# Kernel tuning notes

Measured on AMD Instinct MI355X. Metric: run time of the kernel, lower is better.

## Reference

```python
import jax, jax.numpy as jnp
import numpy as np

N = 4096
C = 8192
D = 64
MARGIN = 0.1
ALPHA = 32.0


def setup_inputs() -> dict:
    key = jax.random.key(0)
    k1, k2, k3, k4 = jax.random.split(key, 4)
    embeddings = jax.random.normal(k1, (N, D), dtype=jnp.float32)
    labels = jax.random.randint(k2, (N,), 0, C)
    # kaiming_normal_(mode='fan_out') on a (C, D) tensor -> std = sqrt(2/C)
    mean_proxies = jax.random.normal(k3, (C, D), dtype=jnp.float32) * np.sqrt(2.0 / C)
    log_variance_proxies = jax.random.normal(k4, (C, D), dtype=jnp.float32) * np.sqrt(2.0 / C)
    return {
        "embeddings": embeddings,
        "labels": labels,
        "mean_proxies": mean_proxies,
        "log_variance_proxies": log_variance_proxies,
    }


def _mls_scores(e, mu, logvar):
    """score[i,j] = -0.5 * sum_d[(e_id - mu_jd)^2 * exp(-logvar_jd) + logvar_jd].
    Expanded into GEMMs to avoid materializing the (N, C, D) broadcast tensor."""
    inv_var = jnp.exp(-logvar)                                  # (C, D)
    e2_term = (e * e) @ inv_var.T                               # (N, C)
    cross = e @ (mu * inv_var).T                                # (N, C)
    const = jnp.sum(mu * mu * inv_var + logvar, axis=1)         # (C,)
    return -0.5 * (e2_term - 2.0 * cross + const[None, :])      # (N, C)


def reference(embeddings, labels, mean_proxies, log_variance_proxies):
    score_mat = _mls_scores(embeddings, mean_proxies, log_variance_proxies)  # (N, C)
    pos_mask = jax.nn.one_hot(labels, C, dtype=score_mat.dtype)              # (N, C)

    pos_e = -ALPHA * (score_mat - MARGIN)
    neg_e = ALPHA * (score_mat + MARGIN)
    m = jnp.max(pos_e)  # NOTE: original code uses max(pos_exp) for BOTH terms
    pos_exp = jnp.exp(pos_e - m)
    neg_exp = jnp.exp(neg_e - m)

    counts = jnp.sum(pos_mask, axis=0)                   # (C,)
    num_valid = jnp.sum(counts != 0).astype(score_mat.dtype)

    pos_sim_sum = jnp.sum(jnp.where(pos_mask == 1, pos_exp, 0.0), axis=0)  # (C,)
    neg_sim_sum = jnp.sum(jnp.where(pos_mask == 0, neg_exp, 0.0), axis=0)  # (C,)

    pos_term = jnp.sum(jnp.log1p(pos_sim_sum) + m) / num_valid
    neg_term = jnp.sum(jnp.log1p(neg_sim_sum) + m) / C
    return pos_term + neg_term
```

## Files before the change

### kernel.cpp

```cpp
#include <hip/hip_runtime.h>
#include <hip/hip_bf16.h>
#include <math.h>


#define N_EMB 4096
#define C_CLS 8192
#define D_DIM 64
#define K_DIM 128

typedef __attribute__((ext_vector_type(8))) __bf16 bf16x8;
typedef __attribute__((ext_vector_type(16))) float f32x16;
typedef __attribute__((ext_vector_type(4))) int i32x4;

__device__ __forceinline__ void async_ld16(void* lds, const void* g) {
  __builtin_amdgcn_global_load_lds(
      (__attribute__((address_space(1))) void*)g,
      (__attribute__((address_space(3))) void*)lds, 16, 0, 0);
}

__global__ void k_prep(const float* __restrict__ emb,
                       const float* __restrict__ mp,
                       const float* __restrict__ lvp,
                       __bf16* __restrict__ wsA,
                       __bf16* __restrict__ wsB,
                       float* __restrict__ constv) {
  int wave = (int)((blockIdx.x * blockDim.x + threadIdx.x) >> 6);
  int lane = threadIdx.x & 63;
  if (wave < N_EMB) {
    float e = emb[wave * D_DIM + lane];
    wsA[wave * K_DIM + lane]         = (__bf16)(e * e);
    wsA[wave * K_DIM + D_DIM + lane] = (__bf16)e;
  } else {
    int j = wave - N_EMB;
    float mu = mp[j * D_DIM + lane];
    float lv = lvp[j * D_DIM + lane];
    float iv = __expf(-lv);
    wsB[j * K_DIM + lane]         = (__bf16)iv;
    wsB[j * K_DIM + D_DIM + lane] = (__bf16)(-2.0f * mu * iv);
    float t = fmaf(mu * mu, iv, lv);
    #pragma unroll
    for (int s = 32; s >= 1; s >>= 1) t += __shfl_xor(t, s);
    if (lane == 0) constv[j] = t;
  }
}

__global__ __launch_bounds__(512, 1) void k_main(
    const __bf16* __restrict__ wsA, const __bf16* __restrict__ wsB,
    const float* __restrict__ constv, const int* __restrict__ labels,
    float* __restrict__ wsM, float* __restrict__ wsP, float* __restrict__ wsN) {
  __shared__ __align__(16) char As[2][32768];
  __shared__ __align__(16) char Bs[32768];

  const int tid = threadIdx.x;
  const int cb = blockIdx.x & 63;
  const int rg = blockIdx.x >> 6;

  const char* Abase = (const char*)wsA + (size_t)rg * 1024 * 256;
  const char* Bg    = (const char*)wsB + (size_t)cb * 128 * 256;

  #pragma unroll
  for (int it = 0; it < 4; ++it) {
    int L = it * 512 + tid;
    int r = L >> 4, cs = L & 15;
    int goff = r * 256 + ((cs ^ (r & 15)) << 4);
    async_ld16(Bs + L * 16, Bg + goff);
  }
  #pragma unroll
  for (int it = 0; it < 4; ++it) {
    int L = it * 512 + tid;
    int r = L >> 4, cs = L & 15;
    int goff = r * 256 + ((cs ^ (r & 15)) << 4);
    async_ld16(As[0] + L * 16, Abase + goff);
  }

  const int wv = tid >> 6, lane = tid & 63;
  const int wc = wv & 1, wr = wv >> 1;
  const int l31 = lane & 31, kg = lane >> 5;
  const int l15 = lane & 15;

  float pcv[2];
  #pragma unroll
  for (int ni = 0; ni < 2; ++ni)
    pcv[ni] = fmaf(16.0f, constv[cb * 128 + wc * 64 + ni * 32 + l31], 3.2f);

  float rM[2] = {-1e30f, -1e30f}, rP[2] = {0.f, 0.f}, rN[2] = {0.f, 0.f};

  __syncthreads();

  for (int t = 0; t < 8; ++t) {
    if (t < 7) {
      const char* Agn = Abase + (size_t)(t + 1) * 32768;
      #pragma unroll
      for (int it = 0; it < 4; ++it) {
        int L = it * 512 + tid;
        int r = L >> 4, cs = L & 15;
        int goff = r * 256 + ((cs ^ (r & 15)) << 4);
        async_ld16(As[(t + 1) & 1] + L * 16, Agn + goff);
      }
    }
    const char* Ac = As[t & 1];

    f32x16 acc[2];
    #pragma unroll
    for (int ni = 0; ni < 2; ++ni)
      #pragma unroll
      for (int r = 0; r < 16; ++r) acc[ni][r] = 0.f;

    #pragma unroll
    for (int kk = 0; kk < 8; ++kk) {
      const int c = kk * 2 + kg;
      const int cofs = (c ^ l15) << 4;
      bf16x8 af = *(const bf16x8*)(Ac + (wr * 32 + l31) * 256 + cofs);
      bf16x8 b0 = *(const bf16x8*)(Bs + (wc * 64 + l31) * 256 + cofs);
      bf16x8 b1 = *(const bf16x8*)(Bs + (wc * 64 + 32 + l31) * 256 + cofs);
      acc[0] = __builtin_amdgcn_mfma_f32_32x32x16_bf16(af, b0, acc[0], 0, 0, 0);
      acc[1] = __builtin_amdgcn_mfma_f32_32x32x16_bf16(af, b1, acc[1], 0, 0, 0);
    }

    const int rowbase = rg * 1024 + t * 128 + wr * 32 + 4 * kg;
    i32x4 labv[4];
    #pragma unroll
    for (int g = 0; g < 4; ++g)
      labv[g] = *(const i32x4*)&labels[rowbase + 8 * g];

    #pragma unroll
    for (int ni = 0; ni < 2; ++ni) {
      const int gcol = cb * 128 + wc * 64 + ni * 32 + l31;
      float lmax = -1e30f;
      #pragma unroll
      for (int r = 0; r < 16; ++r)
        lmax = fmaxf(lmax, fmaf(16.0f, acc[ni][r], pcv[ni]));
      lmax = fmaxf(lmax, __shfl_xor(lmax, 32));
      float ps = 0.f, ns = 0.f;
      #pragma unroll
      for (int r = 0; r < 16; ++r) {
        float pe = fmaf(16.0f, acc[ni][r], pcv[ni]);
        bool match = (labv[r >> 2][r & 3] == gcol);
        float v = match ? pe : (6.4f - pe);
        float ex = __expf(v - lmax);
        ps += match ? ex : 0.f;
        ns += match ? 0.f : ex;
      }
      ps += __shfl_xor(ps, 32);
      ns += __shfl_xor(ns, 32);
      float nM = fmaxf(rM[ni], lmax);
      float sO = __expf(rM[ni] - nM), sN = __expf(lmax - nM);
      rP[ni] = fmaf(rP[ni], sO, ps * sN);
      rN[ni] = fmaf(rN[ni], sO, ns * sN);
      rM[ni] = nM;
    }
    __syncthreads();
  }

  float* colred = (float*)As[0];
  if (kg == 0) {
    #pragma unroll
    for (int ni = 0; ni < 2; ++ni) {
      int cl = wc * 64 + ni * 32 + l31;
      float* cr = &colred[(wr * 128 + cl) * 3];
      cr[0] = rM[ni]; cr[1] = rP[ni]; cr[2] = rN[ni];
    }
  }
  __syncthreads();
  if (tid < 128) {
    float M = -1e30f;
    #pragma unroll
    for (int w = 0; w < 4; ++w) M = fmaxf(M, colred[(w * 128 + tid) * 3]);
    float P = 0.f, Nn = 0.f;
    #pragma unroll
    for (int w = 0; w < 4; ++w) {
      const float* cr = &colred[(w * 128 + tid) * 3];
      float s = __expf(cr[0] - M);
      P = fmaf(cr[1], s, P);
      Nn = fmaf(cr[2], s, Nn);
    }
    int gcol = cb * 128 + tid;
    wsM[rg * C_CLS + gcol] = M;
    wsP[rg * C_CLS + gcol] = P;
    wsN[rg * C_CLS + gcol] = Nn;
  }
}

__global__ __launch_bounds__(1024) void k_fin(
    const float* __restrict__ wsM, const float* __restrict__ wsP,
    const float* __restrict__ wsN, const int* __restrict__ labels,
    float* __restrict__ out) {
  __shared__ unsigned char flag[C_CLS];
  __shared__ float sA[16], sB[16];
  __shared__ int sI[16];
  const int tid = threadIdx.x;
  const int wv = tid >> 6, lane = tid & 63;

  float colM[8], colP[8], colN[8];
  float gm = -1e30f;
  #pragma unroll
  for (int k = 0; k < 8; ++k) {
    int j = k * 1024 + tid;
    float m0 = wsM[0 * C_CLS + j], m1 = wsM[1 * C_CLS + j];
    float m2 = wsM[2 * C_CLS + j], m3 = wsM[3 * C_CLS + j];
    float M = fmaxf(fmaxf(m0, m1), fmaxf(m2, m3));
    float s0 = __expf(m0 - M), s1 = __expf(m1 - M);
    float s2 = __expf(m2 - M), s3 = __expf(m3 - M);
    colM[k] = M;
    colP[k] = fmaf(wsP[0 * C_CLS + j], s0, fmaf(wsP[1 * C_CLS + j], s1,
              fmaf(wsP[2 * C_CLS + j], s2, wsP[3 * C_CLS + j] * s3)));
    colN[k] = fmaf(wsN[0 * C_CLS + j], s0, fmaf(wsN[1 * C_CLS + j], s1,
              fmaf(wsN[2 * C_CLS + j], s2, wsN[3 * C_CLS + j] * s3)));
    gm = fmaxf(gm, M);
  }

  for (int i = tid; i < C_CLS; i += 1024) flag[i] = 0;
  __syncthreads();
  for (int i = tid; i < N_EMB; i += 1024) flag[labels[i]] = 1;
  __syncthreads();
  int nv = 0;
  #pragma unroll
  for (int k = 0; k < 8; ++k) nv += flag[k * 1024 + tid];
  #pragma unroll
  for (int s = 32; s >= 1; s >>= 1) {
    gm = fmaxf(gm, __shfl_xor(gm, s));
    nv += __shfl_xor(nv, s);
  }
  if (lane == 0) { sA[wv] = gm; sI[wv] = nv; }
  __syncthreads();
  if (tid == 0) {
    float mm = -1e30f; int n = 0;
    #pragma unroll
    for (int k = 0; k < 16; ++k) { mm = fmaxf(mm, sA[k]); n += sI[k]; }
    sA[0] = mm; sI[0] = n;
  }
  __syncthreads();
  const float m = sA[0];
  const int num_valid = sI[0];
  __syncthreads();
  float pt = 0.f, nt = 0.f;
  #pragma unroll
  for (int k = 0; k < 8; ++k) {
    float s = __expf(colM[k] - m);
    pt += log1pf(colP[k] * s);
    nt += log1pf(colN[k] * s);
  }
  #pragma unroll
  for (int s = 32; s >= 1; s >>= 1) {
    pt += __shfl_xor(pt, s);
    nt += __shfl_xor(nt, s);
  }
  if (lane == 0) { sA[wv] = pt; sB[wv] = nt; }
  __syncthreads();
  if (tid == 0) {
    float sp = 0.f, sn = 0.f;
    #pragma unroll
    for (int k = 0; k < 16; ++k) { sp += sA[k]; sn += sB[k]; }
    out[0] = (sp + (float)C_CLS * m) / (float)num_valid
           + (sn + (float)C_CLS * m) / (float)C_CLS;
  }
}

extern "C" void kernel_launch(void* const* d_in, const int* in_sizes, int n_in,
                              void* d_out, int out_size, void* d_ws, size_t ws_size,
                              hipStream_t stream) {
  const float* emb    = (const float*)d_in[0];
  const int*   labels = (const int*)d_in[1];
  const float* mp     = (const float*)d_in[2];
  const float* lvp    = (const float*)d_in[3];
  float* out = (float*)d_out;

  char* ws = (char*)d_ws;
  __bf16* wsA   = (__bf16*)ws;
  __bf16* wsB   = (__bf16*)(ws + (1u << 20));
  float* constv = (float*)(ws + 3u * (1u << 20));
  float* wsM    = (float*)(ws + 3u * (1u << 20) + (1u << 15));
  float* wsP    = wsM + 4 * C_CLS;
  float* wsN    = wsP + 4 * C_CLS;

  hipLaunchKernelGGL(k_prep, dim3((N_EMB + C_CLS) / 4), dim3(256), 0, stream,
                     emb, mp, lvp, wsA, wsB, constv);
  hipLaunchKernelGGL(k_main, dim3(4 * (C_CLS / 128)), dim3(512), 0, stream,
                     wsA, wsB, constv, labels, wsM, wsP, wsN);
  hipLaunchKernelGGL(k_fin, dim3(1), dim3(1024), 0, stream,
                     wsM, wsP, wsN, labels, out);
}
```

Before: 104.1 us.

## Split row groups into eight and halve block size for more k_main blocks

```diff
diff --git a/kernel.cpp b/kernel.cpp
--- a/kernel.cpp
+++ b/kernel.cpp
@@ -44,30 +44,30 @@
   }
 }
 
-__global__ __launch_bounds__(512, 1) void k_main(
+__global__ __launch_bounds__(256, 2) void k_main(
     const __bf16* __restrict__ wsA, const __bf16* __restrict__ wsB,
     const float* __restrict__ constv, const int* __restrict__ labels,
     float* __restrict__ wsM, float* __restrict__ wsP, float* __restrict__ wsN) {
-  __shared__ __align__(16) char As[2][32768];
+  __shared__ __align__(16) char As[2][16384];
   __shared__ __align__(16) char Bs[32768];
 
   const int tid = threadIdx.x;
   const int cb = blockIdx.x & 63;
   const int rg = blockIdx.x >> 6;
 
-  const char* Abase = (const char*)wsA + (size_t)rg * 1024 * 256;
+  const char* Abase = (const char*)wsA + (size_t)rg * 512 * 256;
   const char* Bg    = (const char*)wsB + (size_t)cb * 128 * 256;
 
   #pragma unroll
-  for (int it = 0; it < 4; ++it) {
-    int L = it * 512 + tid;
+  for (int it = 0; it < 8; ++it) {
+    int L = it * 256 + tid;
     int r = L >> 4, cs = L & 15;
     int goff = r * 256 + ((cs ^ (r & 15)) << 4);
     async_ld16(Bs + L * 16, Bg + goff);
   }
   #pragma unroll
   for (int it = 0; it < 4; ++it) {
-    int L = it * 512 + tid;
+    int L = it * 256 + tid;
     int r = L >> 4, cs = L & 15;
     int goff = r * 256 + ((cs ^ (r & 15)) << 4);
     async_ld16(As[0] + L * 16, Abase + goff);
@@ -89,10 +89,10 @@
 
   for (int t = 0; t < 8; ++t) {
     if (t < 7) {
-      const char* Agn = Abase + (size_t)(t + 1) * 32768;
+      const char* Agn = Abase + (size_t)(t + 1) * 16384;
       #pragma unroll
       for (int it = 0; it < 4; ++it) {
-        int L = it * 512 + tid;
+        int L = it * 256 + tid;
         int r = L >> 4, cs = L & 15;
         int goff = r * 256 + ((cs ^ (r & 15)) << 4);
         async_ld16(As[(t + 1) & 1] + L * 16, Agn + goff);
@@ -117,7 +117,7 @@
       acc[1] = __builtin_amdgcn_mfma_f32_32x32x16_bf16(af, b1, acc[1], 0, 0, 0);
     }
 
-    const int rowbase = rg * 1024 + t * 128 + wr * 32 + 4 * kg;
+    const int rowbase = rg * 512 + t * 64 + wr * 32 + 4 * kg;
     i32x4 labv[4];
     #pragma unroll
     for (int g = 0; g < 4; ++g)
@@ -163,21 +163,14 @@
   }
   __syncthreads();
   if (tid < 128) {
-    float M = -1e30f;
-    #pragma unroll
-    for (int w = 0; w < 4; ++w) M = fmaxf(M, colred[(w * 128 + tid) * 3]);
-    float P = 0.f, Nn = 0.f;
-    #pragma unroll
-    for (int w = 0; w < 4; ++w) {
-      const float* cr = &colred[(w * 128 + tid) * 3];
-      float s = __expf(cr[0] - M);
-      P = fmaf(cr[1], s, P);
-      Nn = fmaf(cr[2], s, Nn);
-    }
+    const float* c0 = &colred[(0 * 128 + tid) * 3];
+    const float* c1 = &colred[(1 * 128 + tid) * 3];
+    float M = fmaxf(c0[0], c1[0]);
+    float s0 = __expf(c0[0] - M), s1 = __expf(c1[0] - M);
     int gcol = cb * 128 + tid;
     wsM[rg * C_CLS + gcol] = M;
-    wsP[rg * C_CLS + gcol] = P;
-    wsN[rg * C_CLS + gcol] = Nn;
+    wsP[rg * C_CLS + gcol] = fmaf(c0[1], s0, c1[1] * s1);
+    wsN[rg * C_CLS + gcol] = fmaf(c0[2], s0, c1[2] * s1);
   }
 }
 
@@ -196,16 +189,21 @@
   #pragma unroll
   for (int k = 0; k < 8; ++k) {
     int j = k * 1024 + tid;
-    float m0 = wsM[0 * C_CLS + j], m1 = wsM[1 * C_CLS + j];
-    float m2 = wsM[2 * C_CLS + j], m3 = wsM[3 * C_CLS + j];
-    float M = fmaxf(fmaxf(m0, m1), fmaxf(m2, m3));
-    float s0 = __expf(m0 - M), s1 = __expf(m1 - M);
-    float s2 = __expf(m2 - M), s3 = __expf(m3 - M);
-    colM[k] = M;
-    colP[k] = fmaf(wsP[0 * C_CLS + j], s0, fmaf(wsP[1 * C_CLS + j], s1,
-              fmaf(wsP[2 * C_CLS + j], s2, wsP[3 * C_CLS + j] * s3)));
-    colN[k] = fmaf(wsN[0 * C_CLS + j], s0, fmaf(wsN[1 * C_CLS + j], s1,
-              fmaf(wsN[2 * C_CLS + j], s2, wsN[3 * C_CLS + j] * s3)));
+    float M = -1e30f;
+    float mv[8];
+    #pragma unroll
+    for (int rg = 0; rg < 8; ++rg) {
+      mv[rg] = wsM[rg * C_CLS + j];
+      M = fmaxf(M, mv[rg]);
+    }
+    float P = 0.f, Nn = 0.f;
+    #pragma unroll
+    for (int rg = 0; rg < 8; ++rg) {
+      float s = __expf(mv[rg] - M);
+      P = fmaf(wsP[rg * C_CLS + j], s, P);
+      Nn = fmaf(wsN[rg * C_CLS + j], s, Nn);
+    }
+    colM[k] = M; colP[k] = P; colN[k] = Nn;
     gm = fmaxf(gm, M);
   }
 
@@ -270,12 +268,12 @@
   __bf16* wsB   = (__bf16*)(ws + (1u << 20));
   float* constv = (float*)(ws + 3u * (1u << 20));
   float* wsM    = (float*)(ws + 3u * (1u << 20) + (1u << 15));
-  float* wsP    = wsM + 4 * C_CLS;
-  float* wsN    = wsP + 4 * C_CLS;
+  float* wsP    = wsM + 8 * C_CLS;
+  float* wsN    = wsP + 8 * C_CLS;
 
   hipLaunchKernelGGL(k_prep, dim3((N_EMB + C_CLS) / 4), dim3(256), 0, stream,
                      emb, mp, lvp, wsA, wsB, constv);
-  hipLaunchKernelGGL(k_main, dim3(4 * (C_CLS / 128)), dim3(512), 0, stream,
+  hipLaunchKernelGGL(k_main, dim3(8 * (C_CLS / 128)), dim3(256), 0, stream,
                      wsA, wsB, constv, labels, wsM, wsP, wsN);
   hipLaunchKernelGGL(k_fin, dim3(1), dim3(1024), 0, stream,
                      wsM, wsP, wsN, labels, out);
```

Measured after the change: 104.2 us. Within noise of the previous version (+0.1%).
